# Kernel optimization log

Hardware: AMD Instinct MI355X
Metric: run time of the kernel (lower is better)

The kernel has to match this reference:

```python
import jax, jax.numpy as jnp
from jax import lax
import numpy as np

# Layer configuration (from init_kwargs; see FilteringActLayer.__init__)
UP = 2                      # up_factor (temp_rate 32 / in_rate 16)
DOWN = 2                    # down_factor (temp_rate 32 / out_rate 16)
PADDING = (11, 10, 11, 10)  # (px0, px1, py0, py1), derived pad_total = 21
GAIN = float(np.sqrt(2.0))  # lrelu gain used in StyleGAN3
SLOPE = 0.2                 # leaky relu negative slope
CLAMP = 256.0               # activation clamp
UP_TAPS = 12
IN_CUTOFF = 8.0
OUT_CUTOFF = 8.0
IN_HALF_WIDTH = 6.0
OUT_HALF_WIDTH = 6.0
TEMP_FS = 32.0              # max(in_rate, out_rate) * act_upsampling


def _design_lowpass(numtaps, cutoff, width, fs):
    """Replicates scipy.signal.firwin(numtaps, cutoff, width=width, fs=fs)."""
    nyq = fs / 2.0
    # kaiser_atten / kaiser_beta
    atten = 2.285 * (numtaps - 1) * np.pi * (width / nyq) + 7.95
    if atten > 50.0:
        beta = 0.1102 * (atten - 8.7)
    elif atten > 21.0:
        beta = 0.5842 * (atten - 21.0) ** 0.4 + 0.07886 * (atten - 21.0)
    else:
        beta = 0.0
    m = np.arange(numtaps) - (numtaps - 1) / 2.0
    c = cutoff / nyq
    h = c * np.sinc(c * m)
    h = h * np.kaiser(numtaps, beta)
    h = h / np.sum(h)  # unity gain at DC (firwin scale=True)
    return h.astype(np.float32)


def _upfirdn2d_sep(x, f, up, down, pad, gain):
    """Zero-insert upsample by `up`, pad, correlate with separable 1D FIR f
    (applied flipped, i.e. true convolution as in the torch reference),
    then subsample by `down`. x: [N,C,H,W], f: [taps]."""
    N, C, H, W = x.shape
    fr = f[::-1].astype(x.dtype)
    kH = fr.reshape(1, 1, -1, 1)
    kW = fr.reshape(1, 1, 1, -1)
    px0, px1, py0, py1 = pad
    xr = x.reshape(N * C, 1, H, W)
    # lhs_dilation implements the zero-insertion; +up-1 hi-pad accounts for the
    # trailing zeros the torch reference keeps after upsampling.
    xr = lax.conv_general_dilated(xr, kH, window_strides=(down, 1),
                                  padding=((py0, py1 + up - 1), (0, 0)),
                                  lhs_dilation=(up, 1))
    xr = lax.conv_general_dilated(xr, kW, window_strides=(1, down),
                                  padding=((0, 0), (px0, px1 + up - 1)),
                                  lhs_dilation=(1, up))
    Ho, Wo = xr.shape[2], xr.shape[3]
    return xr.reshape(N, C, Ho, Wo) * gain


def setup_inputs() -> dict:
    key = jax.random.key(0)
    k1, k2 = jax.random.split(key)
    x = jax.random.normal(k1, (8, 512, 64, 64), dtype=jnp.float32)
    bias = jax.random.normal(k2, (512,), dtype=jnp.float32) * 0.1
    up_filter = jnp.asarray(_design_lowpass(UP_TAPS, IN_CUTOFF, IN_HALF_WIDTH * 2, TEMP_FS))
    down_filter = jnp.asarray(_design_lowpass(UP_TAPS, OUT_CUTOFF, OUT_HALF_WIDTH * 2, TEMP_FS))
    return {"x": x, "bias": bias, "up_filter": up_filter, "down_filter": down_filter}


def reference(x, bias, up_filter, down_filter):
    # (1) FIR upsample (gain = up^2 to preserve signal magnitude)
    y = _upfirdn2d_sep(x, up_filter, UP, 1, PADDING, float(UP * UP))
    # (2) bias + leaky-relu + gain + clamp (bias_act 'lrelu')
    y = y + bias[None, :, None, None]
    y = jnp.where(y >= 0, y, y * SLOPE) * GAIN
    y = jnp.clip(y, -CLAMP, CLAMP)
    # (3) FIR downsample
    y = _upfirdn2d_sep(y, down_filter, 1, DOWN, (0, 0, 0, 0), 1.0)
    return y
```

## Files before the change

kernel.cpp:

```cpp
#include <hip/hip_runtime.h>

#define SIN 80
#define ST1 80
#define ST3 72

typedef float v2f __attribute__((ext_vector_type(2)));

static __device__ __forceinline__ v2f fma2(v2f a, v2f b, v2f c) {
    return __builtin_elementwise_fma(a, b, c);
}
static __device__ __forceinline__ v2f bcast2(float s) {
    v2f r; r.x = s; r.y = s; return r;
}
static __device__ __forceinline__ v2f mk2(float a, float b) {
    v2f r; r.x = a; r.y = b; return r;
}

__global__ __launch_bounds__(512, 6)
void synth_fused(const float* __restrict__ x, const float* __restrict__ bias,
                 const float* __restrict__ fu, const float* __restrict__ fd,
                 float* __restrict__ out)
{
    __shared__ __align__(16) float bufA[5328];
    __shared__ __align__(16) float bufB[5928];
    __shared__ float sfilt[24];
    float* const s_in = bufA;
    float* const s_t3 = bufA;
    float* const s_t1 = bufB;

    const int tid  = threadIdx.x;
    const int bx   = blockIdx.x;
    const int tile = bx & 1;
    const int nc   = bx >> 1;
    const int gy0  = tile << 5;

    if (tid < 24) sfilt[tid] = (tid < 12) ? fu[tid] : fd[tid - 12];
    const float bc = bias[nc & 511];
    const float* __restrict__ xc = x + ((size_t)nc << 12);

    #pragma unroll
    for (int it = 0; it < 2; ++it) {
        int idx = tid + (it << 9);
        if (idx < 672) {
            int r  = idx >> 4;
            int c4 = (idx & 15) << 2;
            int gy = gy0 - 5 + r;
            float4 v = make_float4(0.f, 0.f, 0.f, 0.f);
            if ((unsigned)gy < 64u)
                v = *reinterpret_cast<const float4*>(xc + (gy << 6) + c4);
            float* dst = s_in + r * SIN + 5 + c4;
            dst[0] = v.x; dst[1] = v.y; dst[2] = v.z; dst[3] = v.w;
        }
    }
    #pragma unroll
    for (int it = 0; it < 2; ++it) {
        int idx = tid + (it << 9);
        if (idx < 672) {
            int r  = idx >> 4;
            int pc = idx & 15;
            int c  = (pc < 5) ? pc : (64 + pc);
            s_in[r * SIN + c] = 0.0f;
        }
    }
    __syncthreads();

    v2f upk[6], gpk[6];
    #pragma unroll
    for (int j = 0; j < 6; ++j) {
        upk[j] = mk2(sfilt[10 - 2*j], sfilt[11 - 2*j]);
        gpk[j] = mk2(sfilt[23 - 2*j], sfilt[22 - 2*j]);
    }

    if (tid < 444) {
        const int g  = tid / 74;
        const int c  = tid - 74 * g;
        const int m0 = 6 * g + (g > 0);
        const float* ip = s_in + m0 * SIN + c;
        float rv[12];
        #pragma unroll
        for (int j = 0; j < 11; ++j) rv[j] = ip[j * SIN];
        rv[11] = (g == 0) ? ip[11 * SIN] : 0.0f;
        float* op = s_t1 + (2 * m0) * ST1 + c;
        #pragma unroll
        for (int mm = 0; mm < 6; ++mm) {
            v2f acc = upk[0] * bcast2(rv[mm]);
            #pragma unroll
            for (int j = 1; j < 6; ++j)
                acc = fma2(upk[j], bcast2(rv[mm + j]), acc);
            op[(2*mm) * ST1]     = acc.x;
            op[(2*mm + 1) * ST1] = acc.y;
        }
        if (g == 0) {
            v2f acc = upk[0] * bcast2(rv[6]);
            #pragma unroll
            for (int j = 1; j < 6; ++j)
                acc = fma2(upk[j], bcast2(rv[6 + j]), acc);
            op[12 * ST1] = acc.x;
            op[13 * ST1] = acc.y;
        }
    }
    __syncthreads();

    const float S42 = 4.0f * 1.41421356237309515f;
    v2f upk2[6];
    #pragma unroll
    for (int j = 0; j < 6; ++j) upk2[j] = upk[j] * S42;
    const float bcs = bc * 1.41421356237309515f;

    if (tid < 444) {
        const int r = tid / 6;
        const int q = tid - 6 * r;
        const float* t1r = s_t1 + r * ST1 + 12 * q;
        float w[22];
        #pragma unroll
        for (int j = 0; j < 11; ++j) {
            v2f v2 = *reinterpret_cast<const v2f*>(t1r + 2 * j);
            w[2*j] = v2.x; w[2*j+1] = v2.y;
        }
        const v2f bc2 = bcast2(bcs);
        v2f t2p[17];
        #pragma unroll
        for (int i = 0; i < 17; ++i) {
            v2f acc = bc2;
            #pragma unroll
            for (int j = 0; j < 6; ++j)
                acc = fma2(upk2[j], bcast2(w[i + j]), acc);
            v2f mx = __builtin_elementwise_max(acc, acc * 0.2f);
            t2p[i] = mk2(__builtin_amdgcn_fmed3f(mx.x, -256.0f, 256.0f),
                         __builtin_amdgcn_fmed3f(mx.y, -256.0f, 256.0f));
        }
        float* t3r = s_t3 + r * ST3 + 12 * q;
        #pragma unroll
        for (int i = 0; i < 3; ++i) {
            float4 o4;
            float* op = &o4.x;
            #pragma unroll
            for (int s = 0; s < 4; ++s) {
                const int oi = 4 * i + s;
                v2f acc = gpk[0] * t2p[oi];
                #pragma unroll
                for (int j = 1; j < 6; ++j) acc = fma2(gpk[j], t2p[oi + j], acc);
                op[s] = acc.x + acc.y;
            }
            *reinterpret_cast<float4*>(t3r + 4 * i) = o4;
        }
    }
    __syncthreads();

    {
        const int c  = tid & 63;
        const int rc = tid >> 6;
        const float* t3c = s_t3 + (rc << 3) * ST3 + c;
        v2f vp[9];
        #pragma unroll
        for (int m = 0; m < 9; ++m)
            vp[m] = mk2(t3c[(2*m) * ST3], t3c[(2*m + 1) * ST3]);
        float* op = out + ((size_t)nc << 12) + ((size_t)(gy0 + (rc << 2)) << 6) + c;
        #pragma unroll
        for (int i = 0; i < 4; ++i) {
            v2f acc = gpk[0] * vp[i];
            #pragma unroll
            for (int j = 1; j < 6; ++j) acc = fma2(gpk[j], vp[i + j], acc);
            op[(size_t)(i << 6)] = acc.x + acc.y;
        }
    }
}

extern "C" void kernel_launch(void* const* d_in, const int* in_sizes, int n_in,
                              void* d_out, int out_size, void* d_ws, size_t ws_size,
                              hipStream_t stream) {
    const float* x    = (const float*)d_in[0];
    const float* bias = (const float*)d_in[1];
    const float* fu   = (const float*)d_in[2];
    const float* fd   = (const float*)d_in[3];
    float* out        = (float*)d_out;

    dim3 grid(8 * 512 * 2);
    dim3 block(512);
    hipLaunchKernelGGL(synth_fused, grid, block, 0, stream, x, bias, fu, fd, out);
}
```

Measured before the change: 153.0 us.

## Interleave row pairs in shared memory to vectorize vertical FIR passes

Restructures the fused upsample/activation/downsample kernel so intermediate buffers store pairs of rows interleaved along columns. Vertical filter passes can then use packed two-wide loads and float4 stores instead of scalar strided accesses. The horizontal stage now does 296 threads processing two rows each with a sliding window of activated values. Occupancy hint is lowered from 6 to 4 waves to allow more registers, which may reduce latency hiding.

```diff
diff --git a/kernel.cpp b/kernel.cpp
--- a/kernel.cpp
+++ b/kernel.cpp
@@ -1,28 +1,24 @@
 #include <hip/hip_runtime.h>
 
-#define SIN 80
-#define ST1 80
-#define ST3 72
+#define SIN  80
+#define ST1I 172
+#define ST3I 132
 
 typedef float v2f __attribute__((ext_vector_type(2)));
 
 static __device__ __forceinline__ v2f fma2(v2f a, v2f b, v2f c) {
     return __builtin_elementwise_fma(a, b, c);
 }
-static __device__ __forceinline__ v2f bcast2(float s) {
-    v2f r; r.x = s; r.y = s; return r;
-}
-static __device__ __forceinline__ v2f mk2(float a, float b) {
-    v2f r; r.x = a; r.y = b; return r;
-}
+static __device__ __forceinline__ v2f bcast2(float s) { v2f r; r.x = s; r.y = s; return r; }
+static __device__ __forceinline__ v2f mk2(float a, float b) { v2f r; r.x = a; r.y = b; return r; }
 
-__global__ __launch_bounds__(512, 6)
+__global__ __launch_bounds__(512, 4)
 void synth_fused(const float* __restrict__ x, const float* __restrict__ bias,
                  const float* __restrict__ fu, const float* __restrict__ fd,
                  float* __restrict__ out)
 {
-    __shared__ __align__(16) float bufA[5328];
-    __shared__ __align__(16) float bufB[5928];
+    __shared__ __align__(16) float bufA[4884];
+    __shared__ __align__(16) float bufB[6364];
     __shared__ float sfilt[24];
     float* const s_in = bufA;
     float* const s_t3 = bufA;
@@ -64,85 +60,96 @@
     }
     __syncthreads();
 
-    v2f upk[6], gpk[6];
+    float u0[12], gs[12];
     #pragma unroll
-    for (int j = 0; j < 6; ++j) {
-        upk[j] = mk2(sfilt[10 - 2*j], sfilt[11 - 2*j]);
-        gpk[j] = mk2(sfilt[23 - 2*j], sfilt[22 - 2*j]);
-    }
+    for (int k = 0; k < 12; ++k) { u0[k] = sfilt[k]; gs[k] = sfilt[23 - k]; }
+    v2f gpk[6];
+    #pragma unroll
+    for (int j = 0; j < 6; ++j) gpk[j] = mk2(gs[2*j], gs[2*j + 1]);
 
     if (tid < 444) {
-        const int g  = tid / 74;
-        const int c  = tid - 74 * g;
-        const int m0 = 6 * g + (g > 0);
-        const float* ip = s_in + m0 * SIN + c;
-        float rv[12];
+        const int g  = tid / 37;
+        const int c2 = tid - 37 * g;
+        const int m0 = 3 * g + (g > 0);
+        const float* ip = s_in + m0 * SIN + 2 * c2;
+        v2f rv[9];
         #pragma unroll
-        for (int j = 0; j < 11; ++j) rv[j] = ip[j * SIN];
-        rv[11] = (g == 0) ? ip[11 * SIN] : 0.0f;
-        float* op = s_t1 + (2 * m0) * ST1 + c;
+        for (int j = 0; j < 8; ++j) rv[j] = *reinterpret_cast<const v2f*>(ip + j * SIN);
+        rv[8] = (g == 0) ? *reinterpret_cast<const v2f*>(ip + 8 * SIN) : bcast2(0.f);
+        float* op = s_t1 + m0 * ST1I + 4 * c2;
         #pragma unroll
-        for (int mm = 0; mm < 6; ++mm) {
-            v2f acc = upk[0] * bcast2(rv[mm]);
+        for (int mm = 0; mm < 3; ++mm) {
+            v2f aE = rv[mm] * u0[10];
+            v2f aO = rv[mm] * u0[11];
             #pragma unroll
-            for (int j = 1; j < 6; ++j)
-                acc = fma2(upk[j], bcast2(rv[mm + j]), acc);
-            op[(2*mm) * ST1]     = acc.x;
-            op[(2*mm + 1) * ST1] = acc.y;
+            for (int j = 1; j < 6; ++j) {
+                aE = fma2(rv[mm + j], bcast2(u0[10 - 2*j]), aE);
+                aO = fma2(rv[mm + j], bcast2(u0[11 - 2*j]), aO);
+            }
+            float4 o4; o4.x = aE.x; o4.y = aO.x; o4.z = aE.y; o4.w = aO.y;
+            *reinterpret_cast<float4*>(op + mm * ST1I) = o4;
         }
         if (g == 0) {
-            v2f acc = upk[0] * bcast2(rv[6]);
+            v2f aE = rv[3] * u0[10];
+            v2f aO = rv[3] * u0[11];
             #pragma unroll
-            for (int j = 1; j < 6; ++j)
-                acc = fma2(upk[j], bcast2(rv[6 + j]), acc);
-            op[12 * ST1] = acc.x;
-            op[13 * ST1] = acc.y;
+            for (int j = 1; j < 6; ++j) {
+                aE = fma2(rv[3 + j], bcast2(u0[10 - 2*j]), aE);
+                aO = fma2(rv[3 + j], bcast2(u0[11 - 2*j]), aO);
+            }
+            float4 o4; o4.x = aE.x; o4.y = aO.x; o4.z = aE.y; o4.w = aO.y;
+            *reinterpret_cast<float4*>(op + 3 * ST1I) = o4;
         }
     }
     __syncthreads();
 
-    const float S42 = 4.0f * 1.41421356237309515f;
-    v2f upk2[6];
-    #pragma unroll
-    for (int j = 0; j < 6; ++j) upk2[j] = upk[j] * S42;
-    const float bcs = bc * 1.41421356237309515f;
+    {
+        const float S42 = 4.0f * 1.41421356237309515f;
+        float us2[12];
+        #pragma unroll
+        for (int k = 0; k < 12; ++k) us2[k] = u0[k] * S42;
+        const float bcs = bc * 1.41421356237309515f;
 
-    if (tid < 444) {
-        const int r = tid / 6;
-        const int q = tid - 6 * r;
-        const float* t1r = s_t1 + r * ST1 + 12 * q;
-        float w[22];
-        #pragma unroll
-        for (int j = 0; j < 11; ++j) {
-            v2f v2 = *reinterpret_cast<const v2f*>(t1r + 2 * j);
-            w[2*j] = v2.x; w[2*j+1] = v2.y;
-        }
-        const v2f bc2 = bcast2(bcs);
-        v2f t2p[17];
-        #pragma unroll
-        for (int i = 0; i < 17; ++i) {
-            v2f acc = bc2;
+        if (tid < 296) {
+            const int rp = tid >> 3;
+            const int q  = tid & 7;
+            const float* t1r = s_t1 + rp * ST1I + 16 * q;
+            v2f wp[18];
             #pragma unroll
-            for (int j = 0; j < 6; ++j)
-                acc = fma2(upk2[j], bcast2(w[i + j]), acc);
-            v2f mx = __builtin_elementwise_max(acc, acc * 0.2f);
-            t2p[i] = mk2(__builtin_amdgcn_fmed3f(mx.x, -256.0f, 256.0f),
-                         __builtin_amdgcn_fmed3f(mx.y, -256.0f, 256.0f));
-        }
-        float* t3r = s_t3 + r * ST3 + 12 * q;
-        #pragma unroll
-        for (int i = 0; i < 3; ++i) {
-            float4 o4;
-            float* op = &o4.x;
+            for (int k = 0; k < 9; ++k) {
+                float4 f4 = *reinterpret_cast<const float4*>(t1r + 4 * k);
+                wp[2*k]   = mk2(f4.x, f4.y);
+                wp[2*k+1] = mk2(f4.z, f4.w);
+            }
+            auto T2 = [&](int m) -> v2f {
+                v2f acc = bcast2(bcs);
+                #pragma unroll
+                for (int j = 0; j < 6; ++j)
+                    acc = fma2(wp[(m >> 1) + j], bcast2(us2[10 + (m & 1) - 2*j]), acc);
+                v2f s2 = acc * 0.2f;
+                return mk2(__builtin_amdgcn_fmed3f(fmaxf(acc.x, s2.x), -256.f, 256.f),
+                           __builtin_amdgcn_fmed3f(fmaxf(acc.y, s2.y), -256.f, 256.f));
+            };
+            v2f t2p[26];
             #pragma unroll
-            for (int s = 0; s < 4; ++s) {
-                const int oi = 4 * i + s;
-                v2f acc = gpk[0] * t2p[oi];
+            for (int m = 0; m < 10; ++m) t2p[m] = T2(m);
+            float* t3r = s_t3 + rp * ST3I + 16 * q;
+            v2f aPrev;
+            #pragma unroll
+            for (int i = 0; i < 8; ++i) {
+                t2p[2*i + 10] = T2(2*i + 10);
+                t2p[2*i + 11] = T2(2*i + 11);
+                v2f a = t2p[2*i] * gs[0];
                 #pragma unroll
-                for (int j = 1; j < 6; ++j) acc = fma2(gpk[j], t2p[oi + j], acc);
-                op[s] = acc.x + acc.y;
+                for (int k = 1; k < 12; ++k)
+                    a = fma2(t2p[2*i + k], bcast2(gs[k]), a);
+                if (i & 1) {
+                    float4 o4; o4.x = aPrev.x; o4.y = aPrev.y; o4.z = a.x; o4.w = a.y;
+                    *reinterpret_cast<float4*>(t3r + 2 * (i - 1)) = o4;
+                } else {
+                    aPrev = a;
+                }
             }
-            *reinterpret_cast<float4*>(t3r + 4 * i) = o4;
         }
     }
     __syncthreads();
@@ -150,18 +157,17 @@
     {
         const int c  = tid & 63;
         const int rc = tid >> 6;
-        const float* t3c = s_t3 + (rc << 3) * ST3 + c;
+        const float* t3c = s_t3 + (rc << 2) * ST3I + 2 * c;
         v2f vp[9];
         #pragma unroll
-        for (int m = 0; m < 9; ++m)
-            vp[m] = mk2(t3c[(2*m) * ST3], t3c[(2*m + 1) * ST3]);
+        for (int j = 0; j < 9; ++j) vp[j] = *reinterpret_cast<const v2f*>(t3c + j * ST3I);
         float* op = out + ((size_t)nc << 12) + ((size_t)(gy0 + (rc << 2)) << 6) + c;
         #pragma unroll
-        for (int i = 0; i < 4; ++i) {
-            v2f acc = gpk[0] * vp[i];
+        for (int s = 0; s < 4; ++s) {
+            v2f acc = vp[s] * gpk[0];
             #pragma unroll
-            for (int j = 1; j < 6; ++j) acc = fma2(gpk[j], vp[i + j], acc);
-            op[(size_t)(i << 6)] = acc.x + acc.y;
+            for (int j = 1; j < 6; ++j) acc = fma2(vp[s + j], gpk[j], acc);
+            op[(size_t)(s << 6)] = acc.x + acc.y;
         }
     }
 }
```

Result: slower. 165.0 us (+7.9%).
